# Kernel tuning notes

Hardware: AMD Instinct MI355X
Metric: run time of the kernel (lower is better)

## Reference

```python
import jax, jax.numpy as jnp
import numpy as np

N_NODES = 60000
N_EDGES = 960000
IN_C = 128
HID = 4 * IN_C       # 512
D_CAT = 8 * IN_C     # 1024
D_FC = 16 * IN_C     # 2048
D_L1 = 32 * IN_C     # 4096
OUT_C = 64
BN_EPS = 1e-5
LEAKY_SLOPE = 0.01


def setup_inputs() -> dict:
    key = jax.random.key(0)
    ks = jax.random.split(key, 32)
    d = {}
    d['x'] = jax.random.normal(ks[0], (N_NODES, IN_C), dtype=jnp.float32)
    d['edge_index'] = jax.random.randint(ks[1], (2, N_EDGES), 0, N_NODES, dtype=jnp.int64)

    def lin(k, fan_in, fan_out):
        k1, k2 = jax.random.split(k)
        bound = 1.0 / np.sqrt(fan_in)
        w = jax.random.uniform(k1, (fan_in, fan_out), jnp.float32, -bound, bound)
        b = jax.random.uniform(k2, (fan_out,), jnp.float32, -bound, bound)
        return w, b

    # GIN conv A MLP: Linear(IN_C,HID) -> BN(HID) -> ReLU -> Linear(HID,HID) -> ReLU
    d['w1a'], d['b1a'] = lin(ks[2], IN_C, HID)
    d['gamma_a'] = jnp.ones((HID,), jnp.float32)
    d['beta_a'] = jnp.zeros((HID,), jnp.float32)
    d['mean_a'] = jax.random.normal(ks[3], (HID,), jnp.float32) * 0.1
    d['var_a'] = jax.random.uniform(ks[4], (HID,), jnp.float32, 0.5, 1.5)
    d['w2a'], d['b2a'] = lin(ks[5], HID, HID)
    # GIN conv B MLP
    d['w1b'], d['b1b'] = lin(ks[6], IN_C, HID)
    d['gamma_b'] = jnp.ones((HID,), jnp.float32)
    d['beta_b'] = jnp.zeros((HID,), jnp.float32)
    d['mean_b'] = jax.random.normal(ks[7], (HID,), jnp.float32) * 0.1
    d['var_b'] = jax.random.uniform(ks[8], (HID,), jnp.float32, 0.5, 1.5)
    d['w2b'], d['b2b'] = lin(ks[9], HID, HID)
    # dense head
    d['fc_w'], d['fc_b'] = lin(ks[10], D_CAT, D_FC)
    d['l1_w'], d['l1_b'] = lin(ks[11], D_FC, D_L1)
    d['l2_w'], d['l2_b'] = lin(ks[12], D_L1, D_FC)
    d['out_w'], d['out_b'] = lin(ks[13], D_FC, OUT_C)
    return d


def _gin_conv(x, edge_index, w1, b1, gamma, beta, mean, var, w2, b2):
    # GINConv, eps=0: h_i = MLP(x_i + sum_{j->i} x_j)
    src, dst = edge_index[0], edge_index[1]
    agg = jax.ops.segment_sum(x[src], dst, num_segments=x.shape[0])
    h = x + agg
    h = h @ w1 + b1
    # BatchNorm1d in eval mode (running stats)
    h = (h - mean) * jax.lax.rsqrt(var + BN_EPS) * gamma + beta
    h = jax.nn.relu(h)
    h = jax.nn.relu(h @ w2 + b2)
    return h


def reference(x, edge_index, w1a, b1a, gamma_a, beta_a, mean_a, var_a, w2a, b2a,
              w1b, b1b, gamma_b, beta_b, mean_b, var_b, w2b, b2b,
              fc_w, fc_b, l1_w, l1_b, l2_w, l2_b, out_w, out_b):
    x1 = _gin_conv(x, edge_index, w1a, b1a, gamma_a, beta_a, mean_a, var_a, w2a, b2a)
    x2 = _gin_conv(x, edge_index, w1b, b1b, gamma_b, beta_b, mean_b, var_b, w2b, b2b)
    h = jnp.concatenate([x1, x2], axis=1)               # [N, 8*in]
    h = jax.nn.leaky_relu(h @ fc_w + fc_b, LEAKY_SLOPE)  # dropout is identity in eval
    h = h @ l1_w + l1_b
    h = h @ l2_w + l2_b
    h = jax.nn.sigmoid(h @ out_w + out_b)
    return h
```

## Files before the change

### kernel.cpp

```cpp
#include <hip/hip_runtime.h>


#define NN 60000
#define NE 960000
#define C_IN 128
#define HID 512
#define DCAT 1024
#define DFC 2048
#define DL1 4096
#define OUTC 64

typedef __bf16 bf16x8 __attribute__((ext_vector_type(8)));
typedef float floatx4 __attribute__((ext_vector_type(4)));

__device__ __forceinline__ unsigned short f2b(float f) {
  unsigned int u = __float_as_uint(f);
  unsigned int r = (u + 0x7fffu + ((u >> 16) & 1u)) >> 16;
  return (unsigned short)r;
}

#define GLOAD_LDS16(g, l)                                                     \
  __builtin_amdgcn_global_load_lds(                                           \
      (__attribute__((address_space(1))) void*)(g),                           \
      (__attribute__((address_space(3))) void*)(l), 16, 0, 0)

__global__ void k_bnparams(const float* __restrict__ g,
                           const float* __restrict__ be,
                           const float* __restrict__ mn,
                           const float* __restrict__ vr,
                           const float* __restrict__ b1,
                           float* __restrict__ scale, float* __restrict__ shift) {
  int i = blockIdx.x * 256 + threadIdx.x;
  if (i < HID) {
    float s = g[i] * rsqrtf(vr[i] + 1e-5f);
    scale[i] = s;
    shift[i] = (b1[i] - mn[i]) * s + be[i];
  }
}

__global__ void k_transpose(const float* __restrict__ in,
                            unsigned short* __restrict__ out, int K, int N) {
  __shared__ float t[32][33];
  int n0 = blockIdx.x * 32, k0 = blockIdx.y * 32;
  int tx = threadIdx.x & 31, ty = threadIdx.x >> 5;
#pragma unroll
  for (int i = 0; i < 32; i += 8)
    t[ty + i][tx] = in[(size_t)(k0 + ty + i) * N + n0 + tx];
  __syncthreads();
#pragma unroll
  for (int i = 0; i < 32; i += 8)
    out[(size_t)(n0 + ty + i) * K + k0 + tx] = f2b(t[tx][ty + i]);
}

__global__ void k_deg(const int* __restrict__ dst, int* __restrict__ deg) {
  int e = blockIdx.x * 256 + threadIdx.x;
  if (e < NE) atomicAdd(&deg[dst[e]], 1);
}

__global__ void k_scan1(const int* __restrict__ deg, int* __restrict__ offs,
                        int* __restrict__ bsum) {
  __shared__ int t[256];
  int i = blockIdx.x * 256 + threadIdx.x;
  int v = (i < NN) ? deg[i] : 0;
  t[threadIdx.x] = v;
  __syncthreads();
#pragma unroll
  for (int d = 1; d < 256; d <<= 1) {
    int add = (threadIdx.x >= d) ? t[threadIdx.x - d] : 0;
    __syncthreads();
    t[threadIdx.x] += add;
    __syncthreads();
  }
  if (i < NN) offs[i] = t[threadIdx.x] - v;
  if (threadIdx.x == 255) bsum[blockIdx.x] = t[255];
}

__global__ void k_scan2(int* __restrict__ bsum, int nb) {
  __shared__ int t[256];
  int v = (threadIdx.x < nb) ? bsum[threadIdx.x] : 0;
  t[threadIdx.x] = v;
  __syncthreads();
#pragma unroll
  for (int d = 1; d < 256; d <<= 1) {
    int add = (threadIdx.x >= d) ? t[threadIdx.x - d] : 0;
    __syncthreads();
    t[threadIdx.x] += add;
    __syncthreads();
  }
  if (threadIdx.x < nb) bsum[threadIdx.x] = t[threadIdx.x] - v;
}

__global__ void k_scan3(int* __restrict__ offs, const int* __restrict__ bsum,
                        int* __restrict__ cursor) {
  int i = blockIdx.x * 256 + threadIdx.x;
  if (i < NN) {
    int o = offs[i] + bsum[blockIdx.x];
    offs[i] = o;
    cursor[i] = o;
  }
  if (i == 0) offs[NN] = NE;
}

__global__ void k_bucket(const int* __restrict__ src, const int* __restrict__ dst,
                         int* __restrict__ cursor, int* __restrict__ esrc) {
  int e = blockIdx.x * 256 + threadIdx.x;
  if (e < NE) {
    int slot = atomicAdd(&cursor[dst[e]], 1);
    esrc[slot] = src[e];
  }
}

__global__ void k_agg(const float2* __restrict__ x2, const int* __restrict__ offs,
                      const int* __restrict__ esrc, unsigned int* __restrict__ h0u) {
  int node = blockIdx.x * 4 + (threadIdx.x >> 6);
  if (node >= NN) return;
  int lane = threadIdx.x & 63;
  int beg = offs[node], end = offs[node + 1];
  float2 acc = x2[(size_t)node * 64 + lane];
  for (int j = beg; j < end; j++) {
    int s = esrc[j];
    float2 v = x2[(size_t)s * 64 + lane];
    acc.x += v.x;
    acc.y += v.y;
  }
  h0u[(size_t)node * 64 + lane] =
      (unsigned)f2b(acc.x) | ((unsigned)f2b(acc.y) << 16);
}

template <int EPI>
__device__ __forceinline__ void gemm_epilogue(
    floatx4 (&acc)[8][4], unsigned short* C, const float* bias,
    const float* scale, const float* shift, int M, int N, int ldc, int m0,
    int n0, int w, int quad, int r16) {
#pragma unroll
  for (int j = 0; j < 4; j++) {
    int gn = n0 + w * 64 + j * 16 + r16;
    int cn = gn < N ? gn : 0;
    float p0, p1 = 0.f;
    if constexpr (EPI == 2) {
      p0 = scale[cn];
      p1 = shift[cn];
    } else {
      p0 = bias[cn];
    }
#pragma unroll
    for (int i = 0; i < 8; i++) {
#pragma unroll
      for (int t = 0; t < 4; t++) {
        int gm = m0 + i * 16 + quad * 4 + t;
        if (gm < M && gn < N) {
          float v = acc[i][j][t];
          if constexpr (EPI == 0) {
            v += p0;
            C[(size_t)gm * ldc + gn] = f2b(v);
          } else if constexpr (EPI == 1) {
            v += p0; v = v > 0.f ? v : 0.f;
            C[(size_t)gm * ldc + gn] = f2b(v);
          } else if constexpr (EPI == 2) {
            v = v * p0 + p1; v = v > 0.f ? v : 0.f;
            C[(size_t)gm * ldc + gn] = f2b(v);
          } else if constexpr (EPI == 3) {
            v += p0; v = v > 0.f ? v : 0.01f * v;
            C[(size_t)gm * ldc + gn] = f2b(v);
          } else {
            v += p0;
            v = 1.f / (1.f + __expf(-v));
            ((float*)C)[(size_t)gm * ldc + gn] = v;
          }
        }
      }
    }
  }
}

__device__ __forceinline__ void gemm_swizzle(int M, int N, int& m0, int& n0) {
  const int mt_total = (M + 127) >> 7, nt_total = (N + 255) >> 8;
  int mt, nt;
  if ((nt_total & 7) == 0) {
    const int ntpx = nt_total >> 3;
    const int x = blockIdx.x & 7;
    const int s = blockIdx.x >> 3;
    nt = x * ntpx + (s % ntpx);
    mt = s / ntpx;
  } else {
    const int GM = 8;
    const int full = (mt_total / GM) * GM;
    const int boundary = full * nt_total;
    int id = blockIdx.x;
    if (id < boundary) {
      int per_group = GM * nt_total;
      int g = id / per_group, r = id % per_group;
      mt = g * GM + r % GM;
      nt = r / GM;
    } else {
      int r = id - boundary, gm = mt_total - full;
      mt = full + r % gm;
      nt = r / gm;
    }
  }
  m0 = mt << 7;
  n0 = nt << 8;
}

__device__ __forceinline__ void gemm_swizzle256(int M, int N, int& m0, int& n0) {
  const int mt_total = (M + 255) >> 8, nt_total = N >> 8;
  int mt, nt;
  if ((nt_total & 7) == 0) {
    const int ntpx = nt_total >> 3;
    const int x = blockIdx.x & 7;
    const int s = blockIdx.x >> 3;
    nt = x * ntpx + (s % ntpx);
    mt = s / ntpx;
  } else {
    const int GM = 8;
    const int full = (mt_total / GM) * GM;
    const int boundary = full * nt_total;
    int id = blockIdx.x;
    if (id < boundary) {
      int per_group = GM * nt_total;
      int g = id / per_group, r = id % per_group;
      mt = g * GM + r % GM;
      nt = r / GM;
    } else {
      int r = id - boundary, gm = mt_total - full;
      mt = full + r % gm;
      nt = r / gm;
    }
  }
  m0 = mt << 8;
  n0 = nt << 8;
}

template <int EPI>
__global__ __launch_bounds__(256, 2) void k_gemm_g(
    const unsigned short* __restrict__ A, const unsigned short* __restrict__ Bt,
    unsigned short* __restrict__ C, const float* __restrict__ bias,
    const float* __restrict__ scale, const float* __restrict__ shift,
    int M, int N, int K, int lda, int ldc) {
  __shared__ __align__(16) unsigned short lsA[4][4][128][8];

  const int tid = threadIdx.x;
  const int w = tid >> 6;
  const int lane = tid & 63;
  const int quad = lane >> 4;
  const int r16 = lane & 15;

  int m0, n0;
  gemm_swizzle(M, N, m0, n0);

  const int ra0 = min(m0 + lane, M - 1);
  const int ra1 = min(m0 + 64 + lane, M - 1);
  const unsigned short* pA0 = A + (size_t)ra0 * lda + w * 8;
  const unsigned short* pA1 = A + (size_t)ra1 * lda + w * 8;
  const unsigned short* pB[4];
#pragma unroll
  for (int j = 0; j < 4; j++) {
    int rb = min(n0 + w * 64 + j * 16 + r16, N - 1);
    pB[j] = Bt + (size_t)rb * K + quad * 8;
  }

  floatx4 acc[8][4];
#pragma unroll
  for (int i = 0; i < 8; i++)
#pragma unroll
    for (int j = 0; j < 4; j++) acc[i][j] = (floatx4){0.f, 0.f, 0.f, 0.f};

  const int niter = K >> 5;

#define ISSUE_A(st)                                                           \
  do {                                                                        \
    GLOAD_LDS16(pA0, &lsA[st][w][0][0]);                                      \
    GLOAD_LDS16(pA1, &lsA[st][w][64][0]);                                     \
    pA0 += 32; pA1 += 32;                                                     \
  } while (0)

  ISSUE_A(0);
  if (niter > 1) ISSUE_A(1);
  if (niter > 2) ISSUE_A(2);
  bf16x8 bcur[4], bnxt[4];
#pragma unroll
  for (int j = 0; j < 4; j++) {
    bcur[j] = *(const bf16x8*)pB[j];
    pB[j] += 32;
  }

  int st = 0;
  for (int t = 0; t < niter; t++) {
    if (t + 2 < niter) {
      asm volatile("s_waitcnt vmcnt(8)\n\ts_barrier" ::: "memory");
    } else if (t + 1 < niter) {
      asm volatile("s_waitcnt vmcnt(6)\n\ts_barrier" ::: "memory");
    } else {
      asm volatile("s_waitcnt vmcnt(4)\n\ts_barrier" ::: "memory");
    }
    if (t + 3 < niter) {
      int s3 = st + 3;
      if (s3 >= 4) s3 -= 4;
      ISSUE_A(s3);
    }
    if (t + 1 < niter) {
#pragma unroll
      for (int j = 0; j < 4; j++) {
        bnxt[j] = *(const bf16x8*)pB[j];
        pB[j] += 32;
      }
    }

    bf16x8 af[8];
#pragma unroll
    for (int i = 0; i < 8; i++)
      af[i] = *(const bf16x8*)&lsA[st][quad][i * 16 + r16][0];
#pragma unroll
    for (int j = 0; j < 4; j++)
#pragma unroll
      for (int i = 0; i < 8; i++)
        acc[i][j] = __builtin_amdgcn_mfma_f32_16x16x32_bf16(af[i], bcur[j],
                                                            acc[i][j], 0, 0, 0);
#pragma unroll
    for (int j = 0; j < 4; j++) bcur[j] = bnxt[j];
    st = (st + 1) & 3;
  }
#undef ISSUE_A

  gemm_epilogue<EPI>(acc, C, bias, scale, shift, M, N, ldc, m0, n0, w, quad, r16);
}

template <int EPI>
__global__ __launch_bounds__(512, 2) void k_gemm8(
    const unsigned short* __restrict__ A, const unsigned short* __restrict__ Bt,
    unsigned short* __restrict__ C, const float* __restrict__ bias,
    const float* __restrict__ scale, const float* __restrict__ shift,
    int M, int N, int K, int lda, int ldc) {
  __shared__ __align__(16) unsigned short smem[2][2][256][64];

  const int tid = threadIdx.x;
  const int w = tid >> 6;
  const int lane = tid & 63;
  const int wm = w >> 2;
  const int wn = w & 3;
  const int quad = lane >> 4;
  const int r16 = lane & 15;

  int m0, n0;
  gemm_swizzle256(M, N, m0, n0);

  const int w8l = w * 8 + (lane >> 3);
  const int csrc = (lane & 7) ^ ((lane >> 3) & 7);
  unsigned offA[2][2], offB[2][2];
#pragma unroll
  for (int h = 0; h < 2; h++)
#pragma unroll
    for (int q = 0; q < 2; q++) {
      int ra = m0 + h * 128 + q * 64 + w8l;
      ra = ra < M ? ra : (M - 1);
      offA[h][q] = (unsigned)ra * (unsigned)(lda * 2) + (unsigned)(csrc * 16);
      int rb = n0 + h * 128 + q * 64 + w8l;
      offB[h][q] = (unsigned)rb * (unsigned)(K * 2) + (unsigned)(csrc * 16);
    }
  const char* Ac = (const char*)A;
  const char* Bc = (const char*)Bt;
  char* smc = (char*)smem;
  const unsigned wdst = (unsigned)(w * 1024);

#define STG_A(T_, h_)                                                          \
  do {                                                                         \
    unsigned kb_ = (unsigned)(T_) * 128u;                                      \
    unsigned db_ = (unsigned)(((T_) & 1) << 16) + (unsigned)((h_) * 16384) + wdst; \
    GLOAD_LDS16(Ac + offA[h_][0] + kb_, smc + db_);                            \
    GLOAD_LDS16(Ac + offA[h_][1] + kb_, smc + db_ + 8192u);                    \
  } while (0)
#define STG_B(T_, h_)                                                          \
  do {                                                                         \
    unsigned kb_ = (unsigned)(T_) * 128u;                                      \
    unsigned db_ = (unsigned)(((T_) & 1) << 16) + 32768u +                     \
                   (unsigned)((h_) * 16384) + wdst;                            \
    GLOAD_LDS16(Bc + offB[h_][0] + kb_, smc + db_);                            \
    GLOAD_LDS16(Bc + offB[h_][1] + kb_, smc + db_ + 8192u);                    \
  } while (0)

  const int swz = r16 & 7;
  const unsigned cK0 = (unsigned)(((quad) ^ swz) * 16);
  const unsigned cK1 = (unsigned)(((4 + quad) ^ swz) * 16);
  const unsigned rdA = (unsigned)((wm * 128 + r16) * 128);
  const unsigned rdB = 32768u + (unsigned)((wn * 64 + r16) * 128);

#define RD_A(bo_, i_, c_) (*(const bf16x8*)(smc + (bo_) + rdA + (unsigned)((i_)*2048) + (c_)))
#define RD_B(bo_, j_, c_) (*(const bf16x8*)(smc + (bo_) + rdB + (unsigned)((j_)*2048) + (c_)))

  floatx4 acc[8][4];
#pragma unroll
  for (int i = 0; i < 8; i++)
#pragma unroll
    for (int j = 0; j < 4; j++) acc[i][j] = (floatx4){0.f, 0.f, 0.f, 0.f};

  const int NT = K >> 6;

  STG_B(0, 0); STG_B(0, 1); STG_A(0, 0); STG_A(0, 1);
  if (NT > 1) {
    STG_B(1, 0); STG_B(1, 1);
    asm volatile("s_waitcnt vmcnt(4)\n\ts_barrier" ::: "memory");
  } else {
    asm volatile("s_waitcnt vmcnt(0)\n\ts_barrier" ::: "memory");
  }

  bf16x8 aF[4][2], bL[2][2], bH[2][2];

  for (int T = 0; T < NT; T++) {
    const unsigned bo = (unsigned)((T & 1) << 16);
#pragma unroll
    for (int i = 0; i < 4; i++) { aF[i][0] = RD_A(bo, i, cK0); aF[i][1] = RD_A(bo, i, cK1); }
#pragma unroll
    for (int j = 0; j < 2; j++) { bL[j][0] = RD_B(bo, j, cK0); bL[j][1] = RD_B(bo, j, cK1); }
    if (T + 1 < NT) STG_A(T + 1, 0);
    asm volatile("s_barrier" ::: "memory");
    asm volatile("s_waitcnt lgkmcnt(0)" ::: "memory");
    __builtin_amdgcn_s_setprio(1);
#pragma unroll
    for (int j = 0; j < 2; j++)
#pragma unroll
      for (int i = 0; i < 4; i++) {
        acc[i][j] = __builtin_amdgcn_mfma_f32_16x16x32_bf16(aF[i][0], bL[j][0], acc[i][j], 0, 0, 0);
        acc[i][j] = __builtin_amdgcn_mfma_f32_16x16x32_bf16(aF[i][1], bL[j][1], acc[i][j], 0, 0, 0);
      }
    __builtin_amdgcn_s_setprio(0);
    asm volatile("s_barrier" ::: "memory");
#pragma unroll
    for (int j = 0; j < 2; j++) { bH[j][0] = RD_B(bo, j + 2, cK0); bH[j][1] = RD_B(bo, j + 2, cK1); }
    if (T + 1 < NT) STG_A(T + 1, 1);
    asm volatile("s_barrier" ::: "memory");
    asm volatile("s_waitcnt lgkmcnt(0)" ::: "memory");
    __builtin_amdgcn_s_setprio(1);
#pragma unroll
    for (int j = 0; j < 2; j++)
#pragma unroll
      for (int i = 0; i < 4; i++) {
        acc[i][j + 2] = __builtin_amdgcn_mfma_f32_16x16x32_bf16(aF[i][0], bH[j][0], acc[i][j + 2], 0, 0, 0);
        acc[i][j + 2] = __builtin_amdgcn_mfma_f32_16x16x32_bf16(aF[i][1], bH[j][1], acc[i][j + 2], 0, 0, 0);
      }
    __builtin_amdgcn_s_setprio(0);
    asm volatile("s_barrier" ::: "memory");
#pragma unroll
    for (int i = 0; i < 4; i++) { aF[i][0] = RD_A(bo, i + 4, cK0); aF[i][1] = RD_A(bo, i + 4, cK1); }
    if (T + 2 < NT) STG_B(T + 2, 0);
    asm volatile("s_barrier" ::: "memory");
    asm volatile("s_waitcnt lgkmcnt(0)" ::: "memory");
    __builtin_amdgcn_s_setprio(1);
#pragma unroll
    for (int j = 0; j < 2; j++)
#pragma unroll
      for (int i = 0; i < 4; i++) {
        acc[i + 4][j + 2] = __builtin_amdgcn_mfma_f32_16x16x32_bf16(aF[i][0], bH[j][0], acc[i + 4][j + 2], 0, 0, 0);
        acc[i + 4][j + 2] = __builtin_amdgcn_mfma_f32_16x16x32_bf16(aF[i][1], bH[j][1], acc[i + 4][j + 2], 0, 0, 0);
      }
    __builtin_amdgcn_s_setprio(0);
    asm volatile("s_barrier" ::: "memory");
    if (T + 2 < NT) STG_B(T + 2, 1);
    asm volatile("s_barrier" ::: "memory");
    __builtin_amdgcn_s_setprio(1);
#pragma unroll
    for (int j = 0; j < 2; j++)
#pragma unroll
      for (int i = 0; i < 4; i++) {
        acc[i + 4][j] = __builtin_amdgcn_mfma_f32_16x16x32_bf16(aF[i][0], bL[j][0], acc[i + 4][j], 0, 0, 0);
        acc[i + 4][j] = __builtin_amdgcn_mfma_f32_16x16x32_bf16(aF[i][1], bL[j][1], acc[i + 4][j], 0, 0, 0);
      }
    __builtin_amdgcn_s_setprio(0);
    if (T + 1 < NT) {
      if (T + 2 < NT) {
        asm volatile("s_waitcnt vmcnt(4)\n\ts_barrier" ::: "memory");
      } else {
        asm volatile("s_waitcnt vmcnt(0)\n\ts_barrier" ::: "memory");
      }
    }
  }
#undef STG_A
#undef STG_B
#undef RD_A
#undef RD_B

  gemm_epilogue<EPI>(acc, C, bias, scale, shift, M, N, ldc, m0 + wm * 128, n0,
                     wn, quad, r16);
}

extern "C" void kernel_launch(void* const* d_in, const int* in_sizes, int n_in,
                              void* d_out, int out_size, void* d_ws,
                              size_t ws_size, hipStream_t stream) {
  typedef const float* cf;
  cf x = (cf)d_in[0];
  const int* ei = (const int*)d_in[1];
  const int* srcI = ei;
  const int* dstI = ei + NE;
  cf w1a = (cf)d_in[2],  b1a = (cf)d_in[3];
  cf ga = (cf)d_in[4],   bea = (cf)d_in[5];
  cf mna = (cf)d_in[6],  vra = (cf)d_in[7];
  cf w2a = (cf)d_in[8],  b2a = (cf)d_in[9];
  cf w1b = (cf)d_in[10], b1b = (cf)d_in[11];
  cf gb = (cf)d_in[12],  beb = (cf)d_in[13];
  cf mnb = (cf)d_in[14], vrb = (cf)d_in[15];
  cf w2b = (cf)d_in[16], b2b = (cf)d_in[17];
  cf fc_w = (cf)d_in[18], fc_b = (cf)d_in[19];
  cf l1_w = (cf)d_in[20], l1_b = (cf)d_in[21];
  cf l2_w = (cf)d_in[22], l2_b = (cf)d_in[23];
  cf ow = (cf)d_in[24],   ob = (cf)d_in[25];
  float* outf = (float*)d_out;

  char* ws = (char*)d_ws;
  size_t off = 0;
  auto carve = [&](size_t bytes) {
    void* p = ws + off;
    off += (bytes + 255) & ~(size_t)255;
    return p;
  };
  unsigned short* wt1ab = (unsigned short*)carve((size_t)DCAT * C_IN * 2);
  unsigned short* wt2a = (unsigned short*)carve((size_t)HID * HID * 2);
  unsigned short* wt2b = (unsigned short*)carve((size_t)HID * HID * 2);
  unsigned short* wtfc = (unsigned short*)carve((size_t)DFC * DCAT * 2);
  unsigned short* wtl1 = (unsigned short*)carve((size_t)DL1 * DFC * 2);
  unsigned short* wtl2 = (unsigned short*)carve((size_t)DFC * DL1 * 2);
  unsigned short* wtout = (unsigned short*)carve((size_t)OUTC * DFC * 2);
  float* scale_ab = (float*)carve(DCAT * 4);
  float* shift_ab = (float*)carve(DCAT * 4);
  unsigned short* h0 = (unsigned short*)carve((size_t)NN * C_IN * 2);

  size_t off_overlay = off;
  int* deg = (int*)carve((size_t)NN * 4);
  int* offs = (int*)carve((size_t)(NN + 1) * 4);
  int* cursor = (int*)carve((size_t)NN * 4);
  int* bsum = (int*)carve(256 * 4);
  int* esrc = (int*)carve((size_t)NE * 4);

  off = off_overlay;
  size_t rem = (ws_size > off + 4096) ? (ws_size - off - 4096) : 0;
  int mchunk = (int)(rem / ((DFC + DL1) * 2));
  if (mchunk > 15104) mchunk = 15104;
  mchunk &= ~127;
  if (mchunk < 128) mchunk = 128;
  unsigned short* bufA = (unsigned short*)carve((size_t)mchunk * DFC * 2);
  unsigned short* bufB = (unsigned short*)carve((size_t)mchunk * DL1 * 2);
  (void)in_sizes; (void)n_in; (void)out_size;

  k_bnparams<<<2, 256, 0, stream>>>(ga, bea, mna, vra, b1a, scale_ab, shift_ab);
  k_bnparams<<<2, 256, 0, stream>>>(gb, beb, mnb, vrb, b1b, scale_ab + HID,
                                    shift_ab + HID);
  k_transpose<<<dim3(HID / 32, C_IN / 32), 256, 0, stream>>>(w1a, wt1ab, C_IN, HID);
  k_transpose<<<dim3(HID / 32, C_IN / 32), 256, 0, stream>>>(
      w1b, wt1ab + (size_t)HID * C_IN, C_IN, HID);
  k_transpose<<<dim3(HID / 32, HID / 32), 256, 0, stream>>>(w2a, wt2a, HID, HID);
  k_transpose<<<dim3(HID / 32, HID / 32), 256, 0, stream>>>(w2b, wt2b, HID, HID);
  k_transpose<<<dim3(DFC / 32, DCAT / 32), 256, 0, stream>>>(fc_w, wtfc, DCAT, DFC);
  k_transpose<<<dim3(DL1 / 32, DFC / 32), 256, 0, stream>>>(l1_w, wtl1, DFC, DL1);
  k_transpose<<<dim3(DFC / 32, DL1 / 32), 256, 0, stream>>>(l2_w, wtl2, DL1, DFC);
  k_transpose<<<dim3(OUTC / 32, DFC / 32), 256, 0, stream>>>(ow, wtout, DFC, OUTC);

  const int NB_NODE = (NN + 255) / 256;
  hipMemsetAsync(deg, 0, (size_t)NN * 4, stream);
  k_deg<<<(NE + 255) / 256, 256, 0, stream>>>(dstI, deg);
  k_scan1<<<NB_NODE, 256, 0, stream>>>(deg, offs, bsum);
  k_scan2<<<1, 256, 0, stream>>>(bsum, NB_NODE);
  k_scan3<<<NB_NODE, 256, 0, stream>>>(offs, bsum, cursor);
  k_bucket<<<(NE + 255) / 256, 256, 0, stream>>>(srcI, dstI, cursor, esrc);
  k_agg<<<(NN + 3) / 4, 256, 0, stream>>>((const float2*)x, offs, esrc,
                                          (unsigned int*)h0);

  auto gemm = [&](int var, int epi, const unsigned short* A,
                  const unsigned short* Bt, unsigned short* Cp, cf bias,
                  const float* sc, const float* sh, int M, int N, int K,
                  int lda, int ldc) {
    if (var == 2) {
      dim3 g(((M + 255) / 256) * (N / 256));
      switch (epi) {
        case 0: k_gemm8<0><<<g, 512, 0, stream>>>(A, Bt, Cp, bias, sc, sh, M, N, K, lda, ldc); break;
        default: k_gemm8<3><<<g, 512, 0, stream>>>(A, Bt, Cp, bias, sc, sh, M, N, K, lda, ldc); break;
      }
    } else {
      dim3 g(((M + 127) / 128) * ((N + 255) / 256));
      switch (epi) {
        case 0: k_gemm_g<0><<<g, 256, 0, stream>>>(A, Bt, Cp, bias, sc, sh, M, N, K, lda, ldc); break;
        case 1: k_gemm_g<1><<<g, 256, 0, stream>>>(A, Bt, Cp, bias, sc, sh, M, N, K, lda, ldc); break;
        case 2: k_gemm_g<2><<<g, 256, 0, stream>>>(A, Bt, Cp, bias, sc, sh, M, N, K, lda, ldc); break;
        case 3: k_gemm_g<3><<<g, 256, 0, stream>>>(A, Bt, Cp, bias, sc, sh, M, N, K, lda, ldc); break;
        default: k_gemm_g<4><<<g, 256, 0, stream>>>(A, Bt, Cp, bias, sc, sh, M, N, K, lda, ldc); break;
      }
    }
  };

  for (int m0 = 0; m0 < NN; m0 += mchunk) {
    const int M = (NN - m0 < mchunk) ? (NN - m0) : mchunk;
    const unsigned short* h0c = h0 + (size_t)m0 * C_IN;
    unsigned short* outc = (unsigned short*)(outf + (size_t)m0 * OUTC);
    gemm(1, 2, h0c, wt1ab, bufA, nullptr, scale_ab, shift_ab, M, DCAT, C_IN, C_IN, DCAT);
    gemm(1, 1, bufA, wt2a, bufB, b2a, nullptr, nullptr, M, HID, HID, DCAT, DCAT);
    gemm(1, 1, bufA + HID, wt2b, bufB + HID, b2b, nullptr, nullptr, M, HID, HID, DCAT, DCAT);
    gemm(2, 3, bufB, wtfc, bufA, fc_b, nullptr, nullptr, M, DFC, DCAT, DCAT, DFC);
    gemm(2, 0, bufA, wtl1, bufB, l1_b, nullptr, nullptr, M, DL1, DFC, DFC, DL1);
    gemm(2, 0, bufB, wtl2, bufA, l2_b, nullptr, nullptr, M, DFC, DL1, DL1, DFC);
    gemm(1, 4, bufA, wtout, outc, ob, nullptr, nullptr, M, OUTC, DFC, DFC, OUTC);
  }
}
```

Before: 3.771 ms.

## Prefetch A tile two stages ahead and stage epilogue through LDS for coalesced stores

The GEMM main loop now issues both A and B tile loads two k-steps ahead, grouped into the third and fourth phases, and waits on vmcnt(8) instead of vmcnt(4). This deepens the global-load pipeline so more memory latency is hidden behind MFMA work. The epilogue applies bias, BN or activation, writes bf16 results into a swizzled per-wave LDS region, then stores full 16-byte rows to global memory for coalescing. Risks are more in-flight loads, correctness of the new wait counts, and an extra LDS round trip in the epilogue.

```diff
diff --git a/kernel.cpp b/kernel.cpp
--- a/kernel.cpp
+++ b/kernel.cpp
@@ -397,8 +397,8 @@
 
   STG_B(0, 0); STG_B(0, 1); STG_A(0, 0); STG_A(0, 1);
   if (NT > 1) {
-    STG_B(1, 0); STG_B(1, 1);
-    asm volatile("s_waitcnt vmcnt(4)\n\ts_barrier" ::: "memory");
+    STG_B(1, 0); STG_B(1, 1); STG_A(1, 0); STG_A(1, 1);
+    asm volatile("s_waitcnt vmcnt(8)\n\ts_barrier" ::: "memory");
   } else {
     asm volatile("s_waitcnt vmcnt(0)\n\ts_barrier" ::: "memory");
   }
@@ -411,7 +411,6 @@
     for (int i = 0; i < 4; i++) { aF[i][0] = RD_A(bo, i, cK0); aF[i][1] = RD_A(bo, i, cK1); }
 #pragma unroll
     for (int j = 0; j < 2; j++) { bL[j][0] = RD_B(bo, j, cK0); bL[j][1] = RD_B(bo, j, cK1); }
-    if (T + 1 < NT) STG_A(T + 1, 0);
     asm volatile("s_barrier" ::: "memory");
     asm volatile("s_waitcnt lgkmcnt(0)" ::: "memory");
     __builtin_amdgcn_s_setprio(1);
@@ -426,7 +425,6 @@
     asm volatile("s_barrier" ::: "memory");
 #pragma unroll
     for (int j = 0; j < 2; j++) { bH[j][0] = RD_B(bo, j + 2, cK0); bH[j][1] = RD_B(bo, j + 2, cK1); }
-    if (T + 1 < NT) STG_A(T + 1, 1);
     asm volatile("s_barrier" ::: "memory");
     asm volatile("s_waitcnt lgkmcnt(0)" ::: "memory");
     __builtin_amdgcn_s_setprio(1);
@@ -441,7 +439,7 @@
     asm volatile("s_barrier" ::: "memory");
 #pragma unroll
     for (int i = 0; i < 4; i++) { aF[i][0] = RD_A(bo, i + 4, cK0); aF[i][1] = RD_A(bo, i + 4, cK1); }
-    if (T + 2 < NT) STG_B(T + 2, 0);
+    if (T + 2 < NT) { STG_B(T + 2, 0); STG_B(T + 2, 1); }
     asm volatile("s_barrier" ::: "memory");
     asm volatile("s_waitcnt lgkmcnt(0)" ::: "memory");
     __builtin_amdgcn_s_setprio(1);
@@ -454,7 +452,7 @@
       }
     __builtin_amdgcn_s_setprio(0);
     asm volatile("s_barrier" ::: "memory");
-    if (T + 2 < NT) STG_B(T + 2, 1);
+    if (T + 2 < NT) { STG_A(T + 2, 0); STG_A(T + 2, 1); }
     asm volatile("s_barrier" ::: "memory");
     __builtin_amdgcn_s_setprio(1);
 #pragma unroll
@@ -467,7 +465,7 @@
     __builtin_amdgcn_s_setprio(0);
     if (T + 1 < NT) {
       if (T + 2 < NT) {
-        asm volatile("s_waitcnt vmcnt(4)\n\ts_barrier" ::: "memory");
+        asm volatile("s_waitcnt vmcnt(8)\n\ts_barrier" ::: "memory");
       } else {
         asm volatile("s_waitcnt vmcnt(0)\n\ts_barrier" ::: "memory");
       }
@@ -478,8 +476,47 @@
 #undef RD_A
 #undef RD_B
 
-  gemm_epilogue<EPI>(acc, C, bias, scale, shift, M, N, ldc, m0 + wm * 128, n0,
-                     wn, quad, r16);
+  __syncthreads();
+  char* eb = smc + (unsigned)(w * 16384);
+#pragma unroll
+  for (int j = 0; j < 4; j++) {
+    int gn = n0 + wn * 64 + j * 16 + r16;
+    float p0 = 0.f, p1 = 0.f;
+    if constexpr (EPI == 2) {
+      p0 = scale[gn];
+      p1 = shift[gn];
+    } else {
+      p0 = bias[gn];
+    }
+#pragma unroll
+    for (int i = 0; i < 8; i++)
+#pragma unroll
+      for (int t = 0; t < 4; t++) {
+        float v = acc[i][j][t];
+        if constexpr (EPI == 0) {
+          v += p0;
+        } else if constexpr (EPI == 1) {
+          v += p0; v = v > 0.f ? v : 0.f;
+        } else if constexpr (EPI == 2) {
+          v = v * p0 + p1; v = v > 0.f ? v : 0.f;
+        } else {
+          v += p0; v = v > 0.f ? v : 0.01f * v;
+        }
+        int row = i * 16 + quad * 4 + t;
+        int col = j * 16 + r16;
+        *(unsigned short*)(eb + row * 128 + (((col >> 3) ^ (row & 7)) << 4) +
+                           ((col & 7) << 1)) = f2b(v);
+      }
+  }
+#pragma unroll
+  for (int r8 = 0; r8 < 16; r8++) {
+    int row = r8 * 8 + (lane >> 3);
+    int chunkG = lane & 7;
+    bf16x8 vv = *(const bf16x8*)(eb + row * 128 + ((chunkG ^ (lane >> 3)) << 4));
+    int gm = m0 + wm * 128 + row;
+    if (gm < M)
+      *(bf16x8*)(C + (size_t)gm * ldc + (n0 + wn * 64 + chunkG * 8)) = vv;
+  }
 }
 
 extern "C" void kernel_launch(void* const* d_in, const int* in_sizes, int n_in,
```

After: 3.279 ms. 1.15x faster.
